# Kernel tuning notes

Measured on AMD Instinct MI355X. Metric: run time of the kernel, lower is better.

The kernel has to match this reference:

```python
import jax, jax.numpy as jnp
import numpy as np

B, S, D, H = 8, 2048, 256, 4
HD = D // H  # 64
EPS = 1e-5


def setup_inputs() -> dict:
    key = jax.random.key(0)
    ks = jax.random.split(key, 16)
    sc = 0.05
    return {
        "descriptors": jax.random.normal(ks[0], (B, S, D), jnp.float32),
        "source": jax.random.normal(ks[1], (B, S, D), jnp.float32),
        "mask": jnp.ones((B, S), jnp.int32),
        # attention projections (stored as [in, out])
        "q_w": jax.random.normal(ks[2], (D, D), jnp.float32) * sc,
        "q_b": jnp.zeros((D,), jnp.float32),
        "k_w": jax.random.normal(ks[3], (D, D), jnp.float32) * sc,
        "k_b": jnp.zeros((D,), jnp.float32),
        "v_w": jax.random.normal(ks[4], (D, D), jnp.float32) * sc,
        "v_b": jnp.zeros((D,), jnp.float32),
        "o_w": jax.random.normal(ks[5], (D, D), jnp.float32) * sc,
        "o_b": jnp.zeros((D,), jnp.float32),
        # MLP layer 0: 2D -> 2D, BatchNorm1d (eval mode) + ReLU
        "m0_w": jax.random.normal(ks[6], (2 * D, 2 * D), jnp.float32) * sc,
        "m0_b": jnp.zeros((2 * D,), jnp.float32),
        "bn_g": jax.random.uniform(ks[7], (2 * D,), jnp.float32, 0.5, 1.5),
        "bn_b": jax.random.normal(ks[8], (2 * D,), jnp.float32) * 0.1,
        "bn_m": jax.random.normal(ks[9], (2 * D,), jnp.float32) * 0.1,
        "bn_v": jax.random.uniform(ks[10], (2 * D,), jnp.float32, 0.5, 1.5),
        # MLP layer 1: 2D -> D, no activation
        "m1_w": jax.random.normal(ks[11], (2 * D, D), jnp.float32) * sc,
        "m1_b": jnp.zeros((D,), jnp.float32),
    }


def reference(descriptors, source, mask, q_w, q_b, k_w, k_b, v_w, v_b, o_w, o_b,
              m0_w, m0_b, bn_g, bn_b, bn_m, bn_v, m1_w, m1_b):
    # Multi-head cross-attention: query=descriptors, key=value=source
    q = (descriptors @ q_w + q_b).reshape(B, S, H, HD).transpose(0, 2, 1, 3)  # [B,H,S,HD]
    k = (source @ k_w + k_b).reshape(B, S, H, HD).transpose(0, 2, 1, 3)
    v = (source @ v_w + v_b).reshape(B, S, H, HD).transpose(0, 2, 1, 3)

    scores = jnp.einsum("bhqd,bhkd->bhqk", q, k) / jnp.sqrt(jnp.float32(HD))
    scores = jnp.where(mask[:, None, None, :] == 0, -1e9, scores)
    probs = jax.nn.softmax(scores.astype(jnp.float32), axis=-1)  # [B,H,S,S]

    ctx = jnp.einsum("bhqk,bhkd->bhqd", probs, v)  # [B,H,S,HD]
    ctx = ctx.transpose(0, 2, 1, 3).reshape(B, S, D)
    attn_out = ctx @ o_w + o_b  # out_proj

    # concat + MLP (Linear -> BatchNorm1d(eval) -> ReLU -> Linear)
    h = jnp.concatenate([descriptors, attn_out], axis=-1)  # [B,S,2D]
    h = h @ m0_w + m0_b
    h = (h - bn_m) * jax.lax.rsqrt(bn_v + EPS) * bn_g + bn_b  # per-channel BN
    h = jax.nn.relu(h)
    h = h @ m1_w + m1_b  # [B,S,D]
    return h
```

## Files before the change

kernel.cpp:

```cpp
#include <hip/hip_runtime.h>

#define NB 8
#define NS 2048
#define ND 256
#define NH 4
#define NHD 64
#define ND2 512
#define NM (NB * NS)
#define C1 0.18033688f

typedef __attribute__((ext_vector_type(8))) short          bf16x8;
typedef __attribute__((ext_vector_type(4))) float          f32x4;
typedef __attribute__((ext_vector_type(16))) float         f32x16;
typedef unsigned short ushort_t;
typedef unsigned int   uint_t;

#define MFMA16(a, b, c) __builtin_amdgcn_mfma_f32_16x16x32_bf16(a, b, c, 0, 0, 0)
#define MFMA32(a, b, c) __builtin_amdgcn_mfma_f32_32x32x16_bf16(a, b, c, 0, 0, 0)

#if __has_builtin(__builtin_amdgcn_exp2f)
#define EXP2(x) __builtin_amdgcn_exp2f(x)
#else
#define EXP2(x) exp2f(x)
#endif

static __device__ inline uint_t pack2bf(float a, float b) {
    union { float f; uint_t u; } x, y; x.f = a; y.f = b;
    return __builtin_amdgcn_perm(y.u + 0x8000u, x.u + 0x8000u, 0x07060302u);
}
static __device__ inline ushort_t f2bf(float f) {
    union { float f; uint_t u; } x; x.f = f;
    return (ushort_t)((x.u + 0x7FFFu + ((x.u >> 16) & 1u)) >> 16);
}
static __device__ inline uint_t cvtpk_bf16(float a, float b) {
    uint_t r;
    asm("v_cvt_pk_bf16_f32 %0, %1, %2" : "=v"(r) : "v"(a), "v"(b));
    return r;
}
static __device__ inline void plswap(uint_t &a, uint_t &b) {
    asm("v_permlane32_swap_b32 %0, %1" : "+v"(a), "+v"(b));
}


static __device__ inline void femit(ushort_t* buf, int n, int k, float v) {
    const int kc = k >> 5;
    const int lane = (((k >> 3) & 3) << 4) | (n & 15);
    const int j = k & 7;
    buf[((size_t)(((n >> 4) * 16 + kc) * 64 + lane)) * 8 + j] = f2bf(v);
}

__global__ __launch_bounds__(256) void prep(
    const float* __restrict__ desc, const float* __restrict__ srcp,
    const int* __restrict__ mask,
    const float* __restrict__ q_w, const float* __restrict__ k_w,
    const float* __restrict__ v_w, const float* __restrict__ m1_w,
    const float* __restrict__ o_w, const float* __restrict__ o_b,
    const float* __restrict__ m0_w, const float* __restrict__ m0_b,
    const float* __restrict__ bng, const float* __restrict__ bnb,
    const float* __restrict__ bnm, const float* __restrict__ bnv,
    ushort_t* __restrict__ descF, ushort_t* __restrict__ srcF,
    ushort_t* __restrict__ qwF, ushort_t* __restrict__ kwF,
    ushort_t* __restrict__ vwF, ushort_t* __restrict__ m1F,
    ushort_t* __restrict__ m0fF, float* __restrict__ biasf,
    float* __restrict__ mbias)
{
    __shared__ float ow[256];
    const int blk = blockIdx.x;
    const int t = threadIdx.x;

    if (blk < 4096) {
        const int y = blk >> 11, x = blk & 2047;
        const float* src = y ? srcp : desc;
        ushort_t* dst    = y ? srcF : descF;
        const int g = x * 256 + t;
        const int lane = g & 63, ci = g >> 6;
        const int kc = ci & 7, r16 = ci >> 3;
        const int row = r16 * 16 + (lane & 15);
        const int c0  = kc * 32 + (lane >> 4) * 8;
        const float* p = src + (size_t)row * ND + c0;
        float4 a = *(const float4*)p;
        float4 b = *(const float4*)(p + 4);
        uint4 pk;
        pk.x = pack2bf(a.x, a.y); pk.y = pack2bf(a.z, a.w);
        pk.z = pack2bf(b.x, b.y); pk.w = pack2bf(b.z, b.w);
        *(uint4*)(dst + (size_t)g * 8) = pk;
    } else if (blk < 4352) {
        const int wb = blk - 4096;
        const int y = wb >> 6, x = wb & 63;
        const float* src; ushort_t* dst; int K, N; float sc = 1.0f;
        switch (y) {
            case 0: src = q_w; dst = qwF; K = 256; N = 256; sc = C1; break;
            case 1: src = k_w; dst = kwF; K = 256; N = 256; break;
            case 2: src = v_w; dst = vwF; K = 256; N = 256; break;
            default: src = m1_w; dst = m1F; K = 512; N = 256; break;
        }
        const int g = x * 256 + t;
        if (g >= (N * K) / 8) return;
        const int lane = g & 63, ci = g >> 6;
        const int lgck = (K == 512) ? 4 : 3;
        const int kc = ci & ((1 << lgck) - 1), n16 = ci >> lgck;
        const int n  = n16 * 16 + (lane & 15);
        const int k0 = kc * 32 + (lane >> 4) * 8;
        float f[8];
#pragma unroll
        for (int j = 0; j < 8; j++) f[j] = src[(size_t)(k0 + j) * N + n] * sc;
        uint4 pk;
        pk.x = pack2bf(f[0], f[1]); pk.y = pack2bf(f[2], f[3]);
        pk.z = pack2bf(f[4], f[5]); pk.w = pack2bf(f[6], f[7]);
        *(uint4*)(dst + (size_t)g * 8) = pk;
    } else if (blk < 4416) {
        const int i = (blk - 4352) * 256 + t;
        mbias[i] = mask[i] ? 0.0f : -1e9f;
    } else if (blk < 4672) {
        const int i = blk - 4416;
        ow[t] = o_w[i * 256 + t];
        __syncthreads();
        float f0 = 0.f, f1 = 0.f;
#pragma unroll 4
        for (int j = 0; j < 256; j++) {
            const float w = ow[j];
            f0 += w * m0_w[(size_t)(256 + j) * 512 + t];
            f1 += w * m0_w[(size_t)(256 + j) * 512 + t + 256];
        }
        const float A0v = bng[t] * rsqrtf(bnv[t] + 1e-5f);
        const float A1v = bng[t + 256] * rsqrtf(bnv[t + 256] + 1e-5f);
        femit(m0fF, t, 256 + i, f0 * A0v);
        femit(m0fF, t + 256, 256 + i, f1 * A1v);
        femit(m0fF, t, i, m0_w[(size_t)i * 512 + t] * A0v);
        femit(m0fF, t + 256, i, m0_w[(size_t)i * 512 + t + 256] * A1v);
    } else {
        const int bb = blk - 4672;
        const int n  = bb * 32 + (t >> 3);
        const int jp = t & 7;
        float s = 0.f;
#pragma unroll 4
        for (int j = jp * 32; j < jp * 32 + 32; j++)
            s += o_b[j] * m0_w[(size_t)(256 + j) * 512 + n];
        s += __shfl_xor(s, 1);
        s += __shfl_xor(s, 2);
        s += __shfl_xor(s, 4);
        if (jp == 0) {
            const float A = bng[n] * rsqrtf(bnv[n] + 1e-5f);
            biasf[n] = (m0_b[n] + s - bnm[n]) * A + bnb[n];
        }
    }
}

template <int KC, int AK, bool NAT, int MT>
static __device__ inline void core(
    const ushort_t* __restrict__ A0, const ushort_t* __restrict__ A1,
    const ushort_t* __restrict__ WF, int t16, int n16, f32x4 acc[MT][4])
{
    const int lane = threadIdx.x & 63;
#pragma unroll
    for (int kc = 0; kc < KC; kc++) {
        const ushort_t* Ab = (kc < AK) ? A0 : A1;
        const int kca = (kc < AK) ? kc : kc - AK;
        bf16x8 af[MT], wf[4];
#pragma unroll
        for (int mt = 0; mt < MT; mt++)
            af[mt] = *(const bf16x8*)(Ab + ((size_t)((t16 + mt) * AK + kca) * 64 + lane) * 8);
#pragma unroll
        for (int nt = 0; nt < 4; nt++)
            wf[nt] = *(const bf16x8*)(WF + ((size_t)((n16 + nt) * KC + kc) * 64 + lane) * 8);
#pragma unroll
        for (int mt = 0; mt < MT; mt++)
#pragma unroll
            for (int nt = 0; nt < 4; nt++) {
                if (NAT) acc[mt][nt] = MFMA16(af[mt], wf[nt], acc[mt][nt]);
                else     acc[mt][nt] = MFMA16(wf[nt], af[mt], acc[mt][nt]);
            }
    }
}

__global__ __launch_bounds__(256) void qkv_frag(
    const ushort_t* __restrict__ descF, const ushort_t* __restrict__ srcF,
    const ushort_t* __restrict__ qwF, const ushort_t* __restrict__ kwF,
    const ushort_t* __restrict__ vwF,
    const float* __restrict__ q_b, const float* __restrict__ k_b,
    const float* __restrict__ v_b,
    ushort_t* __restrict__ qF, ushort_t* __restrict__ kF,
    ushort_t* __restrict__ vF)
{
    const int t = threadIdx.x, w = t >> 6;
    const int lq = t & 15, lg = (t & 63) >> 4;
    const int h    = blockIdx.x;
    const int tok0 = (blockIdx.y << 8) + (w << 6);
    const int t16  = tok0 >> 4, n16 = h << 2;
    const int z    = blockIdx.z;

    f32x4 acc[4][4];
#pragma unroll
    for (int mt = 0; mt < 4; mt++)
#pragma unroll
        for (int nt = 0; nt < 4; nt++) acc[mt][nt] = (f32x4){0.f, 0.f, 0.f, 0.f};

    if (z == 2) {
        core<8, 8, true, 4>(srcF, srcF, vwF, t16, n16, acc);
#pragma unroll
        for (int nt = 0; nt < 4; nt++) {
            const int dvh = nt * 16 + lq;
            const float bs = v_b[h * 64 + dvh];
#pragma unroll
            for (int mt = 0; mt < 4; mt++) {
                const int tok = tok0 + mt * 16 + lg * 4;
                const int b = tok >> 11, s0 = tok & 2047;
                const int bh = b * NH + h;
                uint2 pv;
                pv.x = pack2bf(acc[mt][nt][0] + bs, acc[mt][nt][1] + bs);
                pv.y = pack2bf(acc[mt][nt][2] + bs, acc[mt][nt][3] + bs);
                const size_t e = (size_t)bh * 131072 +
                    ((size_t)((dvh >> 4) * 64 + (s0 >> 5)) * 64 +
                     (((s0 >> 3) & 3) * 16 + (dvh & 15))) * 8 + (s0 & 7);
                *(uint2*)(vF + e) = pv;
            }
        }
    } else {
        const ushort_t* A = z ? srcF : descF;
        const ushort_t* W = z ? kwF : qwF;
        const float* bias = z ? k_b : q_b;
        ushort_t* dst     = z ? kF : qF;
        const float bsc   = z ? 1.0f : C1;
        core<8, 8, false, 4>(A, A, W, t16, n16, acc);
#pragma unroll
        for (int nt = 0; nt < 4; nt++) {
            const int d0 = nt * 16 + lg * 4;
            f32x4 b4 = *(const f32x4*)(bias + h * 64 + d0);
#pragma unroll
            for (int mt = 0; mt < 4; mt++) {
                const int tok = tok0 + mt * 16 + lq;
                const int b = tok >> 11, s = tok & 2047;
                const int bh = b * NH + h;
                uint2 pv;
                pv.x = pack2bf(acc[mt][nt][0] + b4[0] * bsc,
                               acc[mt][nt][1] + b4[1] * bsc);
                pv.y = pack2bf(acc[mt][nt][2] + b4[2] * bsc,
                               acc[mt][nt][3] + b4[3] * bsc);
                const size_t e = (size_t)bh * 131072 +
                    ((size_t)((s >> 4) * 2 + (d0 >> 5)) * 64 +
                     (((d0 >> 3) & 3) * 16 + lq)) * 8 + (d0 & 7);
                *(uint2*)(dst + e) = pv;
            }
        }
    }
}

__global__ __launch_bounds__(256) void mlp0_frag(
    const ushort_t* __restrict__ descF, const ushort_t* __restrict__ ctxF,
    const ushort_t* __restrict__ m0fF, const float* __restrict__ biasf,
    ushort_t* __restrict__ hF)
{
    const int t = threadIdx.x, w = t >> 6;
    const int lq = t & 15, lg = (t & 63) >> 4;
    const int n0   = blockIdx.x << 6;
    const int tok0 = (blockIdx.y << 8) + (w << 6);
    const int t16  = tok0 >> 4, n16 = n0 >> 4;

    f32x4 acc[4][4];
#pragma unroll
    for (int mt = 0; mt < 4; mt++)
#pragma unroll
        for (int nt = 0; nt < 4; nt++) acc[mt][nt] = (f32x4){0.f, 0.f, 0.f, 0.f};

    core<16, 8, false, 4>(descF, ctxF, m0fF, t16, n16, acc);

#pragma unroll
    for (int nt = 0; nt < 4; nt++) {
        const int c0 = n0 + nt * 16 + lg * 4;
        f32x4 b4 = *(const f32x4*)(biasf + c0);
#pragma unroll
        for (int mt = 0; mt < 4; mt++) {
            const int tok = tok0 + mt * 16 + lq;
            uint2 pv;
            pv.x = pack2bf(fmaxf(acc[mt][nt][0] + b4[0], 0.f),
                           fmaxf(acc[mt][nt][1] + b4[1], 0.f));
            pv.y = pack2bf(fmaxf(acc[mt][nt][2] + b4[2], 0.f),
                           fmaxf(acc[mt][nt][3] + b4[3], 0.f));
            const size_t e = ((size_t)((tok >> 4) * 16 + (c0 >> 5)) * 64 +
                              (((c0 >> 3) & 3) * 16 + lq)) * 8 + (c0 & 7);
            *(uint2*)(hF + e) = pv;
        }
    }
}

__global__ __launch_bounds__(256) void mlp1_frag(
    const ushort_t* __restrict__ hF, const ushort_t* __restrict__ m1F,
    const float* __restrict__ m1_b, float* __restrict__ out)
{
    const int t = threadIdx.x, w = t >> 6;
    const int lq = t & 15, lg = (t & 63) >> 4;
    const int n0   = blockIdx.x << 6;
    const int tok0 = (blockIdx.y << 7) + (w << 5);
    const int t16  = tok0 >> 4, n16 = n0 >> 4;

    f32x4 acc[2][4];
#pragma unroll
    for (int mt = 0; mt < 2; mt++)
#pragma unroll
        for (int nt = 0; nt < 4; nt++) acc[mt][nt] = (f32x4){0.f, 0.f, 0.f, 0.f};

    core<16, 16, false, 2>(hF, hF, m1F, t16, n16, acc);

#pragma unroll
    for (int nt = 0; nt < 4; nt++) {
        const int c0 = n0 + nt * 16 + lg * 4;
        f32x4 b4 = *(const f32x4*)(m1_b + c0);
#pragma unroll
        for (int mt = 0; mt < 2; mt++) {
            const int tok = tok0 + mt * 16 + lq;
            f32x4 o4;
#pragma unroll
            for (int j = 0; j < 4; j++) o4[j] = acc[mt][nt][j] + b4[j];
            *(f32x4*)(out + (size_t)tok * ND + c0) = o4;
        }
    }
}

__global__ __launch_bounds__(256) void attn_frag(
    const ushort_t* __restrict__ qF, const ushort_t* __restrict__ kF,
    const ushort_t* __restrict__ vF, const float* __restrict__ mbias,
    ushort_t* __restrict__ ctxF)
{
    const int t = threadIdx.x, w = t >> 6, lane = t & 63;
    const int q = lane & 31, h = lane >> 5;
    const int flat = blockIdx.x + (blockIdx.y << 4) + (blockIdx.z << 6);
    const int bh = (flat & 7) + (((flat >> 7) & 3) << 3);
    const int qb = (flat >> 3) & 15;

    const ushort_t* qh = qF + (size_t)bh * 131072;
    const ushort_t* kh = kF + (size_t)bh * 131072;
    const ushort_t* vh = vF + (size_t)bh * 131072;
    const float* mrow = mbias + (bh >> 2) * NS;

    const int qrow0 = qb * 128 + w * 32;
    const int tok = qrow0 + q;

    bf16x8 qf[4];
#pragma unroll
    for (int st = 0; st < 4; st++)
        qf[st] = *(const bf16x8*)(qh +
            ((size_t)(((tok >> 4) * 2 + (st >> 1)) * 64 +
                      ((st * 2 + h) & 3) * 16 + (tok & 15))) * 8);

    f32x16 o[2];
#pragma unroll
    for (int dt = 0; dt < 2; dt++)
#pragma unroll
        for (int j = 0; j < 16; j++) o[dt][j] = 0.f;
    float l_part = 0.0f;

    bf16x8 ka[2][4];
#pragma unroll
    for (int kt = 0; kt < 2; kt++)
#pragma unroll
        for (int st = 0; st < 4; st++) {
            const int key = kt * 32 + q;
            ka[kt][st] = *(const bf16x8*)(kh +
                ((size_t)(((key >> 4) * 2 + (st >> 1)) * 64 +
                          ((st * 2 + h) & 3) * 16 + (key & 15))) * 8);
        }

    for (int key0 = 0; key0 < NS; key0 += 64) {
        bf16x8 vf[2][4];
#pragma unroll
        for (int dt = 0; dt < 2; dt++)
#pragma unroll
            for (int st = 0; st < 4; st++) {
                const int d = dt * 32 + q;
                vf[dt][st] = *(const bf16x8*)(vh +
                    ((size_t)(((d >> 4) * 64 + (key0 >> 5) + (st >> 1)) * 64 +
                              ((st * 2 + h) & 3) * 16 + (d & 15))) * 8);
            }

        f32x16 sa[2];
#pragma unroll
        for (int kt = 0; kt < 2; kt++)
#pragma unroll
            for (int r1 = 0; r1 < 4; r1++) {
                f32x4 m4 = *(const f32x4*)(mrow + key0 + kt * 32 + r1 * 8 + h * 4);
#pragma unroll
                for (int r0 = 0; r0 < 4; r0++) sa[kt][r1 * 4 + r0] = m4[r0];
            }

        __builtin_amdgcn_s_setprio(1);
#pragma unroll
        for (int kt = 0; kt < 2; kt++)
#pragma unroll
            for (int st = 0; st < 4; st++)
                sa[kt] = MFMA32(ka[kt][st], qf[st], sa[kt]);
        __builtin_amdgcn_s_setprio(0);

        const int keyn = (key0 + 64) & (NS - 1);
#pragma unroll
        for (int kt = 0; kt < 2; kt++)
#pragma unroll
            for (int st = 0; st < 4; st++) {
                const int key = keyn + kt * 32 + q;
                ka[kt][st] = *(const bf16x8*)(kh +
                    ((size_t)(((key >> 4) * 2 + (st >> 1)) * 64 +
                              ((st * 2 + h) & 3) * 16 + (key & 15))) * 8);
            }

        uint_t W[2][4][2];
#pragma unroll
        for (int kt = 0; kt < 2; kt++)
#pragma unroll
            for (int r1 = 0; r1 < 4; r1++)
#pragma unroll
                for (int wv = 0; wv < 2; wv++) {
                    const float p0 = EXP2(sa[kt][r1 * 4 + wv * 2]);
                    const float p1 = EXP2(sa[kt][r1 * 4 + wv * 2 + 1]);
                    l_part += p0 + p1;
                    W[kt][r1][wv] = cvtpk_bf16(p0, p1);
                }
#pragma unroll
        for (int kt = 0; kt < 2; kt++)
#pragma unroll
            for (int s1 = 0; s1 < 2; s1++)
#pragma unroll
                for (int wv = 0; wv < 2; wv++)
                    plswap(W[kt][2 * s1][wv], W[kt][2 * s1 + 1][wv]);

        __builtin_amdgcn_s_setprio(1);
#pragma unroll
        for (int st = 0; st < 4; st++) {
            const int kt = st >> 1, s1 = st & 1;
            union { uint_t u[4]; bf16x8 v; } pb;
            pb.u[0] = W[kt][2 * s1][0];
            pb.u[1] = W[kt][2 * s1][1];
            pb.u[2] = W[kt][2 * s1 + 1][0];
            pb.u[3] = W[kt][2 * s1 + 1][1];
#pragma unroll
            for (int dt = 0; dt < 2; dt++)
                o[dt] = MFMA32(vf[dt][st], pb.v, o[dt]);
        }
        __builtin_amdgcn_s_setprio(0);
    }

    l_part += __shfl_xor(l_part, 32);
    const float li = 1.0f / l_part;

    const int tok16 = (bh >> 2) * 128 + (tok >> 4);
#pragma unroll
    for (int dt = 0; dt < 2; dt++)
#pragma unroll
        for (int r1 = 0; r1 < 4; r1++) {
            const int c = (bh & 3) * 64 + dt * 32 + r1 * 8 + h * 4;
            uint2 pv;
            pv.x = cvtpk_bf16(o[dt][r1 * 4 + 0] * li, o[dt][r1 * 4 + 1] * li);
            pv.y = cvtpk_bf16(o[dt][r1 * 4 + 2] * li, o[dt][r1 * 4 + 3] * li);
            const size_t e = ((size_t)(tok16 * 8 + (c >> 5)) * 64 +
                              (((c >> 3) & 3) * 16 + (tok & 15))) * 8 + (c & 7);
            *(uint2*)(ctxF + e) = pv;
        }
}

extern "C" void kernel_launch(void* const* d_in, const int* in_sizes, int n_in,
                              void* d_out, int out_size, void* d_ws, size_t ws_size,
                              hipStream_t stream)
{
    (void)in_sizes; (void)n_in; (void)out_size; (void)ws_size;
    const float* desc = (const float*)d_in[0];
    const float* srcp = (const float*)d_in[1];
    const int*   mask = (const int*)d_in[2];
    const float* q_w  = (const float*)d_in[3];
    const float* q_b  = (const float*)d_in[4];
    const float* k_w  = (const float*)d_in[5];
    const float* k_b  = (const float*)d_in[6];
    const float* v_w  = (const float*)d_in[7];
    const float* v_b  = (const float*)d_in[8];
    const float* o_w  = (const float*)d_in[9];
    const float* o_b  = (const float*)d_in[10];
    const float* m0_w = (const float*)d_in[11];
    const float* m0_b = (const float*)d_in[12];
    const float* bng  = (const float*)d_in[13];
    const float* bnb  = (const float*)d_in[14];
    const float* bnm  = (const float*)d_in[15];
    const float* bnv  = (const float*)d_in[16];
    const float* m1_w = (const float*)d_in[17];
    const float* m1_b = (const float*)d_in[18];
    float* out = (float*)d_out;

    const size_t ASZ = (size_t)NM * ND;
    ushort_t* descF = (ushort_t*)d_ws;
    ushort_t* srcF  = descF + ASZ;
    ushort_t* qF    = descF + 2 * ASZ;
    ushort_t* kF    = descF + 3 * ASZ;
    ushort_t* vF    = descF + 4 * ASZ;
    ushort_t* qwF   = descF + 5 * ASZ;
    ushort_t* kwF   = qwF + 65536;
    ushort_t* vwF   = kwF + 65536;
    ushort_t* m1F   = vwF + 65536;
    ushort_t* m0fF  = m1F + 131072;
    float*    biasf = (float*)(m0fF + 262144);
    float*    mbias = biasf + 512;
    ushort_t* ctxF  = srcF;
    ushort_t* hF    = qF;

    const dim3 blk(256);

    prep<<<dim3(4688), blk, 0, stream>>>(
        desc, srcp, mask, q_w, k_w, v_w, m1_w, o_w, o_b, m0_w, m0_b,
        bng, bnb, bnm, bnv, descF, srcF, qwF, kwF, vwF, m1F, m0fF, biasf, mbias);

    qkv_frag<<<dim3(4, NM / 256, 3), blk, 0, stream>>>(
        descF, srcF, qwF, kwF, vwF, q_b, k_b, v_b, qF, kF, vF);
    attn_frag<<<dim3(NS / 128, NH, NB), blk, 0, stream>>>(qF, kF, vF, mbias, ctxF);
    mlp0_frag<<<dim3(8, NM / 256), blk, 0, stream>>>(descF, ctxF, m0fF, biasf, hF);
    mlp1_frag<<<dim3(4, NM / 128), blk, 0, stream>>>(hF, m1F, m1_b, out);
}
```

Baseline: 243.5 us.

## Stage K/V tiles through double-buffered LDS via direct global-to-LDS loads

The attention kernel previously had each of its 4 waves load its own K and V fragments from global memory into registers. Now the block cooperatively copies each 64-key K/V tile into a double-buffered shared-memory buffer using global_load_lds, prefetching the next tile while computing the current one. Each wave then reads its fragments from LDS. This cuts redundant global traffic across waves, but adds a block-wide barrier every iteration and LDS read latency. There is also no explicit vmcnt wait before the barrier, so correctness relies on the compiler inserting one.

```diff
diff --git a/kernel.cpp b/kernel.cpp
--- a/kernel.cpp
+++ b/kernel.cpp
@@ -39,6 +39,11 @@
 }
 static __device__ inline void plswap(uint_t &a, uint_t &b) {
     asm("v_permlane32_swap_b32 %0, %1" : "+v"(a), "+v"(b));
+}
+static __device__ inline void gl2lds16(const ushort_t* g, ushort_t* l) {
+    __builtin_amdgcn_global_load_lds(
+        (const __attribute__((address_space(1))) void*)g,
+        (__attribute__((address_space(3))) void*)l, 16, 0, 0);
 }
 
 
@@ -321,8 +326,12 @@
     const ushort_t* __restrict__ vF, const float* __restrict__ mbias,
     ushort_t* __restrict__ ctxF)
 {
+    __shared__ ushort_t Kb[2][4096];
+    __shared__ ushort_t Vb[2][4096];
+
     const int t = threadIdx.x, w = t >> 6, lane = t & 63;
     const int q = lane & 31, h = lane >> 5;
+    const int qlo = q & 15, qhi = q >> 4;
     const int flat = blockIdx.x + (blockIdx.y << 4) + (blockIdx.z << 6);
     const int bh = (flat & 7) + (((flat >> 7) & 3) << 3);
     const int qb = (flat >> 3) & 15;
@@ -342,6 +351,15 @@
             ((size_t)(((tok >> 4) * 2 + (st >> 1)) * 64 +
                       ((st * 2 + h) & 3) * 16 + (tok & 15))) * 8);
 
+    {
+        const ushort_t* kg = kh + (w << 10) + (lane << 3);
+        gl2lds16(kg,       &Kb[0][(w << 10)]);
+        gl2lds16(kg + 512, &Kb[0][(w << 10) + 512]);
+        const ushort_t* vg = vh + ((size_t)(w * 64) << 9) + (lane << 3);
+        gl2lds16(vg,       &Vb[0][(w << 10)]);
+        gl2lds16(vg + 512, &Vb[0][(w << 10) + 512]);
+    }
+
     f32x16 o[2];
 #pragma unroll
     for (int dt = 0; dt < 2; dt++)
@@ -349,28 +367,11 @@
         for (int j = 0; j < 16; j++) o[dt][j] = 0.f;
     float l_part = 0.0f;
 
-    bf16x8 ka[2][4];
-#pragma unroll
-    for (int kt = 0; kt < 2; kt++)
-#pragma unroll
-        for (int st = 0; st < 4; st++) {
-            const int key = kt * 32 + q;
-            ka[kt][st] = *(const bf16x8*)(kh +
-                ((size_t)(((key >> 4) * 2 + (st >> 1)) * 64 +
-                          ((st * 2 + h) & 3) * 16 + (key & 15))) * 8);
-        }
+    __syncthreads();
 
     for (int key0 = 0; key0 < NS; key0 += 64) {
-        bf16x8 vf[2][4];
-#pragma unroll
-        for (int dt = 0; dt < 2; dt++)
-#pragma unroll
-            for (int st = 0; st < 4; st++) {
-                const int d = dt * 32 + q;
-                vf[dt][st] = *(const bf16x8*)(vh +
-                    ((size_t)(((d >> 4) * 64 + (key0 >> 5) + (st >> 1)) * 64 +
-                              ((st * 2 + h) & 3) * 16 + (d & 15))) * 8);
-            }
+        const int c  = (key0 >> 6) & 1;
+        const int cn = c ^ 1;
 
         f32x16 sa[2];
 #pragma unroll
@@ -382,24 +383,39 @@
                 for (int r0 = 0; r0 < 4; r0++) sa[kt][r1 * 4 + r0] = m4[r0];
             }
 
+        {
+            const int keyn = (key0 + 64) & (NS - 1);
+            const ushort_t* kg = kh + ((size_t)(keyn >> 4) << 10) + (w << 10) + (lane << 3);
+            gl2lds16(kg,       &Kb[cn][(w << 10)]);
+            gl2lds16(kg + 512, &Kb[cn][(w << 10) + 512]);
+            const ushort_t* vg = vh + ((size_t)(w * 64 + (keyn >> 5)) << 9) + (lane << 3);
+            gl2lds16(vg,       &Vb[cn][(w << 10)]);
+            gl2lds16(vg + 512, &Vb[cn][(w << 10) + 512]);
+        }
+
+        bf16x8 kfr[2][4], vfr[2][4];
+#pragma unroll
+        for (int kt = 0; kt < 2; kt++)
+#pragma unroll
+            for (int st = 0; st < 4; st++)
+                kfr[kt][st] = *(const bf16x8*)&Kb[c][
+                    ((((kt * 2 + qhi) * 2 + (st >> 1))) << 9) +
+                    (((st * 2 + h) & 3) << 7) + (qlo << 3)];
+#pragma unroll
+        for (int dt = 0; dt < 2; dt++)
+#pragma unroll
+            for (int st = 0; st < 4; st++)
+                vfr[dt][st] = *(const bf16x8*)&Vb[c][
+                    ((((dt * 2 + qhi) * 2 + (st >> 1))) << 9) +
+                    (((st * 2 + h) & 3) << 7) + (qlo << 3)];
+
         __builtin_amdgcn_s_setprio(1);
 #pragma unroll
         for (int kt = 0; kt < 2; kt++)
 #pragma unroll
             for (int st = 0; st < 4; st++)
-                sa[kt] = MFMA32(ka[kt][st], qf[st], sa[kt]);
+                sa[kt] = MFMA32(kfr[kt][st], qf[st], sa[kt]);
         __builtin_amdgcn_s_setprio(0);
-
-        const int keyn = (key0 + 64) & (NS - 1);
-#pragma unroll
-        for (int kt = 0; kt < 2; kt++)
-#pragma unroll
-            for (int st = 0; st < 4; st++) {
-                const int key = keyn + kt * 32 + q;
-                ka[kt][st] = *(const bf16x8*)(kh +
-                    ((size_t)(((key >> 4) * 2 + (st >> 1)) * 64 +
-                              ((st * 2 + h) & 3) * 16 + (key & 15))) * 8);
-            }
 
         uint_t W[2][4][2];
 #pragma unroll
@@ -432,9 +448,11 @@
             pb.u[3] = W[kt][2 * s1 + 1][1];
 #pragma unroll
             for (int dt = 0; dt < 2; dt++)
-                o[dt] = MFMA32(vf[dt][st], pb.v, o[dt]);
+                o[dt] = MFMA32(vfr[dt][st], pb.v, o[dt]);
         }
         __builtin_amdgcn_s_setprio(0);
+
+        __syncthreads();
     }
 
     l_part += __shfl_xor(l_part, 32);
```

Result: no change. 246.9 us (+1.4%).

## Split attention key range across two wave groups and merge partials in LDS

Applied to the files above, without the earlier changes.

The attention kernel now launches 512 threads per block. Two groups of four waves each process half of the key sequence for the same query rows. The second group writes its unnormalized output accumulators and row sums to shared memory, and the first group adds them before normalizing and storing. This doubles the waves per block so more parallel work can hide latency. It relies on the softmax having no running-max subtraction, so the partials add directly. The cost is about 32KB of LDS, a block barrier, and a tighter register budget from launch_bounds(512,4).

```diff
diff --git a/kernel.cpp b/kernel.cpp
--- a/kernel.cpp
+++ b/kernel.cpp
@@ -316,12 +316,16 @@
     }
 }
 
-__global__ __launch_bounds__(256) void attn_frag(
+__global__ __launch_bounds__(512, 4) void attn_frag(
     const ushort_t* __restrict__ qF, const ushort_t* __restrict__ kF,
     const ushort_t* __restrict__ vF, const float* __restrict__ mbias,
     ushort_t* __restrict__ ctxF)
 {
+    __shared__ f32x4 Ob[4][2][4][64];
+    __shared__ float Ls[4][64];
+
     const int t = threadIdx.x, w = t >> 6, lane = t & 63;
+    const int wq = w & 3, kw = w >> 2;
     const int q = lane & 31, h = lane >> 5;
     const int flat = blockIdx.x + (blockIdx.y << 4) + (blockIdx.z << 6);
     const int bh = (flat & 7) + (((flat >> 7) & 3) << 3);
@@ -332,8 +336,9 @@
     const ushort_t* vh = vF + (size_t)bh * 131072;
     const float* mrow = mbias + (bh >> 2) * NS;
 
-    const int qrow0 = qb * 128 + w * 32;
+    const int qrow0 = qb * 128 + wq * 32;
     const int tok = qrow0 + q;
+    const int kbase = kw << 10;
 
     bf16x8 qf[4];
 #pragma unroll
@@ -354,13 +359,15 @@
     for (int kt = 0; kt < 2; kt++)
 #pragma unroll
         for (int st = 0; st < 4; st++) {
-            const int key = kt * 32 + q;
+            const int key = kbase + kt * 32 + q;
             ka[kt][st] = *(const bf16x8*)(kh +
                 ((size_t)(((key >> 4) * 2 + (st >> 1)) * 64 +
                           ((st * 2 + h) & 3) * 16 + (key & 15))) * 8);
         }
 
-    for (int key0 = 0; key0 < NS; key0 += 64) {
+    for (int k0 = 0; k0 < 1024; k0 += 64) {
+        const int key0 = kbase + k0;
+
         bf16x8 vf[2][4];
 #pragma unroll
         for (int dt = 0; dt < 2; dt++)
@@ -390,7 +397,7 @@
                 sa[kt] = MFMA32(ka[kt][st], qf[st], sa[kt]);
         __builtin_amdgcn_s_setprio(0);
 
-        const int keyn = (key0 + 64) & (NS - 1);
+        const int keyn = kbase + ((k0 + 64) & 1023);
 #pragma unroll
         for (int kt = 0; kt < 2; kt++)
 #pragma unroll
@@ -438,17 +445,36 @@
     }
 
     l_part += __shfl_xor(l_part, 32);
-    const float li = 1.0f / l_part;
+
+    if (kw) {
+#pragma unroll
+        for (int dt = 0; dt < 2; dt++)
+#pragma unroll
+            for (int r1 = 0; r1 < 4; r1++) {
+                f32x4 v;
+#pragma unroll
+                for (int r0 = 0; r0 < 4; r0++) v[r0] = o[dt][r1 * 4 + r0];
+                Ob[wq][dt][r1][lane] = v;
+            }
+        Ls[wq][lane] = l_part;
+    }
+    __syncthreads();
+    if (kw) return;
+
+    const float li = 1.0f / (l_part + Ls[wq][lane]);
 
     const int tok16 = (bh >> 2) * 128 + (tok >> 4);
 #pragma unroll
     for (int dt = 0; dt < 2; dt++)
 #pragma unroll
         for (int r1 = 0; r1 < 4; r1++) {
+            const f32x4 p = Ob[wq][dt][r1][lane];
             const int c = (bh & 3) * 64 + dt * 32 + r1 * 8 + h * 4;
             uint2 pv;
-            pv.x = cvtpk_bf16(o[dt][r1 * 4 + 0] * li, o[dt][r1 * 4 + 1] * li);
-            pv.y = cvtpk_bf16(o[dt][r1 * 4 + 2] * li, o[dt][r1 * 4 + 3] * li);
+            pv.x = cvtpk_bf16((o[dt][r1 * 4 + 0] + p[0]) * li,
+                              (o[dt][r1 * 4 + 1] + p[1]) * li);
+            pv.y = cvtpk_bf16((o[dt][r1 * 4 + 2] + p[2]) * li,
+                              (o[dt][r1 * 4 + 3] + p[3]) * li);
             const size_t e = ((size_t)(tok16 * 8 + (c >> 5)) * 64 +
                               (((c >> 3) & 3) * 16 + (tok & 15))) * 8 + (c & 7);
             *(uint2*)(ctxF + e) = pv;
@@ -505,7 +531,7 @@
 
     qkv_frag<<<dim3(4, NM / 256, 3), blk, 0, stream>>>(
         descF, srcF, qwF, kwF, vwF, q_b, k_b, v_b, qF, kF, vF);
-    attn_frag<<<dim3(NS / 128, NH, NB), blk, 0, stream>>>(qF, kF, vF, mbias, ctxF);
+    attn_frag<<<dim3(NS / 128, NH, NB), dim3(512), 0, stream>>>(qF, kF, vF, mbias, ctxF);
     mlp0_frag<<<dim3(8, NM / 256), blk, 0, stream>>>(descF, ctxF, m0fF, biasf, hF);
     mlp1_frag<<<dim3(4, NM / 128), blk, 0, stream>>>(hF, m1F, m1_b, out);
 }
```

Result: slower. 339.8 us (+39.6%).
